# Performance work log

Measured on AMD Instinct MI355X. Metric: run time of the kernel, lower is better.

Reference implementation:

```python
import jax, jax.numpy as jnp
import numpy as np
import math

B, T, D, H = 4, 2048, 1024, 16
DH = D // H

def setup_inputs() -> dict:
    key = jax.random.key(0)
    k1, k2, k3, k4, k5 = jax.random.split(key, 5)
    s = 1.0 / math.sqrt(D)
    x = jax.random.normal(k1, (B, T, D), dtype=jnp.float32)
    # causal mask: 1 where attention allowed (j <= i), 0 elsewhere
    mask = jnp.tril(jnp.ones((T, T), dtype=jnp.float32))[None, None, :, :]
    W_qkv = jax.random.normal(k2, (D, 3 * D), dtype=jnp.float32) * s
    b_qkv = jax.random.normal(k3, (3 * D,), dtype=jnp.float32) * 0.02
    W_proj = jax.random.normal(k4, (D, D), dtype=jnp.float32) * s
    b_proj = jax.random.normal(k5, (D,), dtype=jnp.float32) * 0.02
    return {"x": x, "mask": mask, "W_qkv": W_qkv, "b_qkv": b_qkv,
            "W_proj": W_proj, "b_proj": b_proj}

def reference(x, mask, W_qkv, b_qkv, W_proj, b_proj):
    # qkv: [B,T,3D] -> [3,B,H,T,DH]
    qkv = x @ W_qkv + b_qkv
    qkv = qkv.reshape(B, T, 3, H, DH).transpose(2, 0, 3, 1, 4)
    q, k, v = qkv[0], qkv[1], qkv[2]
    scores = jnp.einsum('bhqd,bhkd->bhqk', q, k) / math.sqrt(DH)
    scores = jnp.where(mask == 0, -jnp.inf, scores)
    attn = jax.nn.softmax(scores, axis=-1)  # dropout p=0 -> identity
    out = jnp.einsum('bhqk,bhkd->bhqd', attn, v)
    out = out.transpose(0, 2, 1, 3).reshape(B, T, D)
    return out @ W_proj + b_proj
```

## Files before the change

### kernel.cpp

```cpp
#include <hip/hip_runtime.h>
#include <hip/hip_bf16.h>

typedef __attribute__((ext_vector_type(8))) short short8;
typedef __attribute__((ext_vector_type(4))) float f32x4;
typedef __attribute__((ext_vector_type(16))) float f32x16;
typedef __attribute__((ext_vector_type(4))) unsigned int u32x4;

#define DEV static __device__ __forceinline__

DEV unsigned short bfc(float f) {
    __bf16 h = (__bf16)f;
    return __builtin_bit_cast(unsigned short, h);
}

DEV unsigned int pack2bf(float lo, float hi) {
    return (unsigned int)bfc(lo) | ((unsigned int)bfc(hi) << 16);
}

DEV void gload16(const void* g, void* l) {
    __builtin_amdgcn_global_load_lds(
        (const __attribute__((address_space(1))) unsigned int*)g,
        (__attribute__((address_space(3))) unsigned int*)l, 16, 0, 0);
}

__global__ void cvt_bf16_kernel(const float* __restrict__ in,
                                unsigned short* __restrict__ out, int n4) {
    int stride = gridDim.x * blockDim.x;
    for (int i = blockIdx.x * blockDim.x + threadIdx.x; i < n4; i += stride) {
        float4 v = reinterpret_cast<const float4*>(in)[i];
        ushort4 o;
        o.x = bfc(v.x); o.y = bfc(v.y); o.z = bfc(v.z); o.w = bfc(v.w);
        reinterpret_cast<ushort4*>(out)[i] = o;
    }
}

__global__ void transpose_cvt_kernel(const float* __restrict__ in,
                                     unsigned short* __restrict__ out,
                                     int K, int N) {
    __shared__ float tile[32][33];
    int n0 = blockIdx.x * 32, k0 = blockIdx.y * 32;
    int tx = threadIdx.x & 31, ty = threadIdx.x >> 5;
    #pragma unroll
    for (int i = 0; i < 32; i += 8)
        tile[ty + i][tx] = in[(size_t)(k0 + ty + i) * N + n0 + tx];
    __syncthreads();
    #pragma unroll
    for (int i = 0; i < 32; i += 8)
        out[(size_t)(n0 + ty + i) * K + k0 + tx] = bfc(tile[tx][ty + i]);
}

template <int EPI>
__global__ __launch_bounds__(256) void gemm_bt(
    const unsigned short* __restrict__ A,
    const unsigned short* __restrict__ Bt,
    const float* __restrict__ bias,
    unsigned short* __restrict__ oQ,
    unsigned short* __restrict__ oK,
    unsigned short* __restrict__ oVt,
    float* __restrict__ oP,
    int M, int N, int K) {
    __shared__ unsigned short As[128 * 32];
    __shared__ unsigned short Bs[128 * 32];
    const int tid = threadIdx.x;
    const int wid = tid >> 6, lane = tid & 63;
    const int r = lane & 15, g = lane >> 4;
    const int wm = wid >> 1, wn = wid & 1;
    const int bm = blockIdx.x, bn = blockIdx.y;

    f32x4 acc[4][4];
    #pragma unroll
    for (int i = 0; i < 4; i++)
        #pragma unroll
        for (int j = 0; j < 4; j++) acc[i][j] = (f32x4)(0.f);

    const int nk = K >> 5;
    for (int kt = 0; kt < nk; ++kt) {
        const int k0 = kt << 5;
        __syncthreads();
        #pragma unroll
        for (int it = 0; it < 2; ++it) {
            int c = it * 256 + wid * 64 + lane;
            int row = c >> 2, cc = c & 3;
            int ccs = cc ^ ((row >> 1) & 3);
            gload16(A + (size_t)(bm * 128 + row) * K + k0 + ccs * 8,
                    (char*)As + (it * 256 + wid * 64) * 16);
            gload16(Bt + (size_t)(bn * 128 + row) * K + k0 + ccs * 8,
                    (char*)Bs + (it * 256 + wid * 64) * 16);
        }
        __syncthreads();
        short8 af[4], bfr[4];
        #pragma unroll
        for (int mi = 0; mi < 4; ++mi) {
            int row = wm * 64 + mi * 16 + r;
            af[mi] = *(const short8*)((const char*)As + row * 64 +
                                      ((g ^ ((row >> 1) & 3)) << 4));
        }
        #pragma unroll
        for (int ni = 0; ni < 4; ++ni) {
            int row = wn * 64 + ni * 16 + r;
            bfr[ni] = *(const short8*)((const char*)Bs + row * 64 +
                                       ((g ^ ((row >> 1) & 3)) << 4));
        }
        #pragma unroll
        for (int mi = 0; mi < 4; ++mi)
            #pragma unroll
            for (int ni = 0; ni < 4; ++ni)
                acc[mi][ni] = __builtin_amdgcn_mfma_f32_16x16x32_bf16(
                    af[mi], bfr[ni], acc[mi][ni], 0, 0, 0);
    }

    const float QSCALE = 0.125f;
    #pragma unroll
    for (int ni = 0; ni < 4; ++ni) {
        int n = bn * 128 + wn * 64 + ni * 16 + r;
        float bb = bias[n];
        #pragma unroll
        for (int mi = 0; mi < 4; ++mi) {
            #pragma unroll
            for (int rr = 0; rr < 4; ++rr) {
                int m = bm * 128 + wm * 64 + mi * 16 + g * 4 + rr;
                float v = acc[mi][ni][rr] + bb;
                if (EPI == 0) {
                    int b = m >> 11, t = m & 2047;
                    int s = n >> 10, hh = (n >> 6) & 15, dh = n & 63;
                    size_t bh = (size_t)(b * 16 + hh);
                    if (s == 0)      oQ[(bh * 2048 + t) * 64 + dh] = bfc(v * QSCALE);
                    else if (s == 1) oK[(bh * 2048 + t) * 64 + dh] = bfc(v);
                    else             oVt[(bh * 64 + dh) * 2048 + t] = bfc(v);
                } else {
                    oP[(size_t)m * N + n] = v;
                }
            }
        }
    }
}

__global__ __launch_bounds__(256) void attn_kernel(
    const unsigned short* __restrict__ Q,
    const unsigned short* __restrict__ Kb,
    const unsigned short* __restrict__ Vt,
    unsigned short* __restrict__ O) {
    __shared__ unsigned short Ks[2 * 64 * 64];
    __shared__ unsigned short Vs[2 * 64 * 64];
    const int tid = threadIdx.x, wid = tid >> 6, lane = tid & 63;
    const int ln31 = lane & 31, hi = lane >> 5;

    const int l = blockIdx.y * 16 + blockIdx.x;
    const int u = l & 255, v = l >> 8;
    const int bh = v * 16 + (u >> 4);
    const int qt = (v & 1) ? (15 - (u & 15)) : (u & 15);

    const size_t hoff = (size_t)bh * 2048 * 64;
    const int qrow0 = qt * 128 + wid * 32;
    const int tq = qrow0 + ln31;
    const float NEG_INF = -__builtin_inff();

    short8 qf[4];
    #pragma unroll
    for (int st = 0; st < 4; ++st)
        qf[st] = *(const short8*)(Q + hoff + (size_t)tq * 64 + st * 16 + hi * 8);

    f32x16 oacc[2];
    oacc[0] = (f32x16)(0.f); oacc[1] = (f32x16)(0.f);
    float mrow = NEG_INF, lrow = 0.f;

    auto stage = [&](int buf, int kvb) {
        #pragma unroll
        for (int it = 0; it < 2; ++it) {
            int c = it * 256 + wid * 64 + lane;
            int row = c >> 3, cc = c & 7;
            int ccs = cc ^ (row & 7);
            gload16(Kb + hoff + (size_t)(kvb + row) * 64 + ccs * 8,
                    (char*)Ks + buf * 8192 + (it * 256 + wid * 64) * 16);
            gload16(Vt + hoff + (size_t)row * 2048 + kvb + ccs * 8,
                    (char*)Vs + buf * 8192 + (it * 256 + wid * 64) * 16);
        }
    };

    const int nkv = 2 * qt + 2;
    stage(0, 0);
    for (int kv = 0; kv < nkv; ++kv) {
        const int kvb = kv * 64;
        const int cur = kv & 1;
        __syncthreads();
        if (kv + 1 < nkv) stage(cur ^ 1, kvb + 64);

        if (kvb <= qrow0) {
            const char* Kbase = (const char*)Ks + cur * 8192;
            const char* Vbase = (const char*)Vs + cur * 8192;
            f32x16 s0 = (f32x16)(0.f), s1 = (f32x16)(0.f);
            #pragma unroll
            for (int st = 0; st < 4; ++st) {
                int row0 = ln31, row1 = 32 + ln31;
                short8 kf0 = *(const short8*)(Kbase + row0 * 128 +
                                              (((2 * st + hi) ^ (row0 & 7)) << 4));
                short8 kf1 = *(const short8*)(Kbase + row1 * 128 +
                                              (((2 * st + hi) ^ (row1 & 7)) << 4));
                s0 = __builtin_amdgcn_mfma_f32_32x32x16_bf16(kf0, qf[st], s0, 0, 0, 0);
                s1 = __builtin_amdgcn_mfma_f32_32x32x16_bf16(kf1, qf[st], s1, 0, 0, 0);
            }
            if (kvb + 63 > qrow0) {
                const int lim = tq - kvb;
                #pragma unroll
                for (int j = 0; j < 16; ++j) {
                    int krel = (j & 3) + 8 * (j >> 2) + 4 * hi;
                    if (krel > lim)      s0[j] = NEG_INF;
                    if (krel + 32 > lim) s1[j] = NEG_INF;
                }
            }
            float mloc = NEG_INF;
            #pragma unroll
            for (int j = 0; j < 16; ++j)
                mloc = fmaxf(mloc, fmaxf(s0[j], s1[j]));
            mloc = fmaxf(mloc, __shfl_xor(mloc, 32));
            float mnew = fmaxf(mrow, mloc);
            float alpha = __expf(mrow - mnew);
            mrow = mnew;
            float ls = 0.f;
            #pragma unroll
            for (int j = 0; j < 16; ++j) {
                float p0 = __expf(s0[j] - mnew);
                float p1 = __expf(s1[j] - mnew);
                s0[j] = p0; s1[j] = p1;
                ls += p0 + p1;
            }
            ls += __shfl_xor(ls, 32);
            lrow = lrow * alpha + ls;
            #pragma unroll
            for (int j = 0; j < 16; ++j) { oacc[0][j] *= alpha; oacc[1][j] *= alpha; }

            #pragma unroll
            for (int m = 0; m < 4; ++m) {
                const int h = m & 1;
                float pa0, pa1, pb0, pb1, pc0, pc1, pd0, pd1;
                if (m < 2) {
                    pa0 = s0[8*h+0]; pa1 = s0[8*h+1]; pc0 = s0[8*h+2]; pc1 = s0[8*h+3];
                    pb0 = s0[8*h+4]; pb1 = s0[8*h+5]; pd0 = s0[8*h+6]; pd1 = s0[8*h+7];
                } else {
                    pa0 = s1[8*h+0]; pa1 = s1[8*h+1]; pc0 = s1[8*h+2]; pc1 = s1[8*h+3];
                    pb0 = s1[8*h+4]; pb1 = s1[8*h+5]; pd0 = s1[8*h+6]; pd1 = s1[8*h+7];
                }
                unsigned int pkA = pack2bf(pa0, pa1), pkC = pack2bf(pc0, pc1);
                unsigned int pkB = pack2bf(pb0, pb1), pkD = pack2bf(pd0, pd1);
                unsigned int oA = __shfl_xor(pkA, 32), oB = __shfl_xor(pkB, 32);
                unsigned int oC = __shfl_xor(pkC, 32), oD = __shfl_xor(pkD, 32);
                u32x4 w;
                w.x = hi ? oB : pkA;
                w.y = hi ? oD : pkC;
                w.z = hi ? pkB : oA;
                w.w = hi ? pkD : oC;
                short8 pfrag = __builtin_bit_cast(short8, w);
                #pragma unroll
                for (int d = 0; d < 2; ++d) {
                    int row = d * 32 + ln31;
                    short8 vf = *(const short8*)(Vbase + row * 128 +
                                                 (((2 * m + hi) ^ (row & 7)) << 4));
                    oacc[d] = __builtin_amdgcn_mfma_f32_32x32x16_bf16(vf, pfrag, oacc[d], 0, 0, 0);
                }
            }
        }
    }

    const int b = bh >> 4, h = bh & 15;
    const float rinv = 1.0f / lrow;
    unsigned short* orow = O + (size_t)(b * 2048 + tq) * 1024 + h * 64;
    #pragma unroll
    for (int d = 0; d < 2; ++d)
        #pragma unroll
        for (int u2 = 0; u2 < 4; ++u2) {
            int dh0 = d * 32 + u2 * 8 + 4 * hi;
            uint2 w;
            w.x = pack2bf(oacc[d][4*u2+0] * rinv, oacc[d][4*u2+1] * rinv);
            w.y = pack2bf(oacc[d][4*u2+2] * rinv, oacc[d][4*u2+3] * rinv);
            *(uint2*)(orow + dh0) = w;
        }
}

extern "C" void kernel_launch(void* const* d_in, const int* in_sizes, int n_in,
                              void* d_out, int out_size, void* d_ws, size_t ws_size,
                              hipStream_t stream) {
    const float* x     = (const float*)d_in[0];
    const float* Wqkv  = (const float*)d_in[2];
    const float* bqkv  = (const float*)d_in[3];
    const float* Wproj = (const float*)d_in[4];
    const float* bproj = (const float*)d_in[5];
    float* out = (float*)d_out;

    char* ws = (char*)d_ws;
    unsigned short* xb  = (unsigned short*)(ws);
    unsigned short* Ob  = (unsigned short*)(ws);
    unsigned short* WqT = (unsigned short*)(ws + (16u << 20));
    unsigned short* WpT = (unsigned short*)(ws + (22u << 20));
    unsigned short* Qb  = (unsigned short*)(ws + (24u << 20));
    unsigned short* Kb  = (unsigned short*)(ws + (40u << 20));
    unsigned short* Vt  = (unsigned short*)(ws + (56u << 20));

    cvt_bf16_kernel<<<2048, 256, 0, stream>>>(x, xb, (8192 * 1024) / 4);
    transpose_cvt_kernel<<<dim3(96, 32), 256, 0, stream>>>(Wqkv, WqT, 1024, 3072);
    transpose_cvt_kernel<<<dim3(32, 32), 256, 0, stream>>>(Wproj, WpT, 1024, 1024);
    gemm_bt<0><<<dim3(64, 24), 256, 0, stream>>>(xb, WqT, bqkv, Qb, Kb, Vt, nullptr,
                                                 8192, 3072, 1024);
    attn_kernel<<<dim3(16, 64), 256, 0, stream>>>(Qb, Kb, Vt, Ob);
    gemm_bt<1><<<dim3(64, 8), 256, 0, stream>>>(Ob, WpT, bproj, nullptr, nullptr,
                                                nullptr, out, 8192, 1024, 1024);
}
```

Baseline: 240.6 us.

## Load K/V fragments directly from global memory, dropping LDS staging and barriers

```diff
diff --git a/kernel.cpp b/kernel.cpp
--- a/kernel.cpp
+++ b/kernel.cpp
@@ -140,8 +140,6 @@
     const unsigned short* __restrict__ Kb,
     const unsigned short* __restrict__ Vt,
     unsigned short* __restrict__ O) {
-    __shared__ unsigned short Ks[2 * 64 * 64];
-    __shared__ unsigned short Vs[2 * 64 * 64];
     const int tid = threadIdx.x, wid = tid >> 6, lane = tid & 63;
     const int ln31 = lane & 31, hi = lane >> 5;
 
@@ -164,100 +162,91 @@
     oacc[0] = (f32x16)(0.f); oacc[1] = (f32x16)(0.f);
     float mrow = NEG_INF, lrow = 0.f;
 
-    auto stage = [&](int buf, int kvb) {
-        #pragma unroll
-        for (int it = 0; it < 2; ++it) {
-            int c = it * 256 + wid * 64 + lane;
-            int row = c >> 3, cc = c & 7;
-            int ccs = cc ^ (row & 7);
-            gload16(Kb + hoff + (size_t)(kvb + row) * 64 + ccs * 8,
-                    (char*)Ks + buf * 8192 + (it * 256 + wid * 64) * 16);
-            gload16(Vt + hoff + (size_t)row * 2048 + kvb + ccs * 8,
-                    (char*)Vs + buf * 8192 + (it * 256 + wid * 64) * 16);
-        }
-    };
-
-    const int nkv = 2 * qt + 2;
-    stage(0, 0);
-    for (int kv = 0; kv < nkv; ++kv) {
+    const unsigned short* Kh = Kb + hoff;
+    const unsigned short* Vh = Vt + hoff;
+
+    const int nt = 2 * qt + (wid >> 1) + 1;
+    for (int kv = 0; kv < nt; ++kv) {
         const int kvb = kv * 64;
-        const int cur = kv & 1;
-        __syncthreads();
-        if (kv + 1 < nkv) stage(cur ^ 1, kvb + 64);
-
-        if (kvb <= qrow0) {
-            const char* Kbase = (const char*)Ks + cur * 8192;
-            const char* Vbase = (const char*)Vs + cur * 8192;
-            f32x16 s0 = (f32x16)(0.f), s1 = (f32x16)(0.f);
-            #pragma unroll
-            for (int st = 0; st < 4; ++st) {
-                int row0 = ln31, row1 = 32 + ln31;
-                short8 kf0 = *(const short8*)(Kbase + row0 * 128 +
-                                              (((2 * st + hi) ^ (row0 & 7)) << 4));
-                short8 kf1 = *(const short8*)(Kbase + row1 * 128 +
-                                              (((2 * st + hi) ^ (row1 & 7)) << 4));
-                s0 = __builtin_amdgcn_mfma_f32_32x32x16_bf16(kf0, qf[st], s0, 0, 0, 0);
-                s1 = __builtin_amdgcn_mfma_f32_32x32x16_bf16(kf1, qf[st], s1, 0, 0, 0);
+
+        const unsigned short* Kp = Kh + (size_t)kvb * 64;
+        short8 kf0[4], kf1[4];
+        #pragma unroll
+        for (int st = 0; st < 4; ++st) {
+            kf0[st] = *(const short8*)(Kp + ln31 * 64 + st * 16 + hi * 8);
+            kf1[st] = *(const short8*)(Kp + (32 + ln31) * 64 + st * 16 + hi * 8);
+        }
+
+        f32x16 s0 = (f32x16)(0.f), s1 = (f32x16)(0.f);
+        #pragma unroll
+        for (int st = 0; st < 4; ++st) {
+            s0 = __builtin_amdgcn_mfma_f32_32x32x16_bf16(kf0[st], qf[st], s0, 0, 0, 0);
+            s1 = __builtin_amdgcn_mfma_f32_32x32x16_bf16(kf1[st], qf[st], s1, 0, 0, 0);
+        }
+
+        short8 vf[4][2];
+        #pragma unroll
+        for (int m = 0; m < 4; ++m)
+            #pragma unroll
+            for (int d = 0; d < 2; ++d)
+                vf[m][d] = *(const short8*)(Vh + (size_t)(d * 32 + ln31) * 2048 +
+                                            kvb + m * 16 + hi * 8);
+
+        if (kvb + 63 > qrow0) {
+            const int lim = tq - kvb;
+            #pragma unroll
+            for (int j = 0; j < 16; ++j) {
+                int krel = (j & 3) + 8 * (j >> 2) + 4 * hi;
+                if (krel > lim)      s0[j] = NEG_INF;
+                if (krel + 32 > lim) s1[j] = NEG_INF;
             }
-            if (kvb + 63 > qrow0) {
-                const int lim = tq - kvb;
-                #pragma unroll
-                for (int j = 0; j < 16; ++j) {
-                    int krel = (j & 3) + 8 * (j >> 2) + 4 * hi;
-                    if (krel > lim)      s0[j] = NEG_INF;
-                    if (krel + 32 > lim) s1[j] = NEG_INF;
-                }
+        }
+
+        float mloc = NEG_INF;
+        #pragma unroll
+        for (int j = 0; j < 16; ++j)
+            mloc = fmaxf(mloc, fmaxf(s0[j], s1[j]));
+        mloc = fmaxf(mloc, __shfl_xor(mloc, 32));
+        float mnew = fmaxf(mrow, mloc);
+        float alpha = __expf(mrow - mnew);
+        mrow = mnew;
+        float ls = 0.f;
+        #pragma unroll
+        for (int j = 0; j < 16; ++j) {
+            float p0 = __expf(s0[j] - mnew);
+            float p1 = __expf(s1[j] - mnew);
+            s0[j] = p0; s1[j] = p1;
+            ls += p0 + p1;
+        }
+        ls += __shfl_xor(ls, 32);
+        lrow = lrow * alpha + ls;
+        #pragma unroll
+        for (int j = 0; j < 16; ++j) { oacc[0][j] *= alpha; oacc[1][j] *= alpha; }
+
+        #pragma unroll
+        for (int m = 0; m < 4; ++m) {
+            const int h = m & 1;
+            float pa0, pa1, pb0, pb1, pc0, pc1, pd0, pd1;
+            if (m < 2) {
+                pa0 = s0[8*h+0]; pa1 = s0[8*h+1]; pc0 = s0[8*h+2]; pc1 = s0[8*h+3];
+                pb0 = s0[8*h+4]; pb1 = s0[8*h+5]; pd0 = s0[8*h+6]; pd1 = s0[8*h+7];
+            } else {
+                pa0 = s1[8*h+0]; pa1 = s1[8*h+1]; pc0 = s1[8*h+2]; pc1 = s1[8*h+3];
+                pb0 = s1[8*h+4]; pb1 = s1[8*h+5]; pd0 = s1[8*h+6]; pd1 = s1[8*h+7];
             }
-            float mloc = NEG_INF;
-            #pragma unroll
-            for (int j = 0; j < 16; ++j)
-                mloc = fmaxf(mloc, fmaxf(s0[j], s1[j]));
-            mloc = fmaxf(mloc, __shfl_xor(mloc, 32));
-            float mnew = fmaxf(mrow, mloc);
-            float alpha = __expf(mrow - mnew);
-            mrow = mnew;
-            float ls = 0.f;
-            #pragma unroll
-            for (int j = 0; j < 16; ++j) {
-                float p0 = __expf(s0[j] - mnew);
-                float p1 = __expf(s1[j] - mnew);
-                s0[j] = p0; s1[j] = p1;
-                ls += p0 + p1;
-            }
-            ls += __shfl_xor(ls, 32);
-            lrow = lrow * alpha + ls;
-            #pragma unroll
-            for (int j = 0; j < 16; ++j) { oacc[0][j] *= alpha; oacc[1][j] *= alpha; }
-
-            #pragma unroll
-            for (int m = 0; m < 4; ++m) {
-                const int h = m & 1;
-                float pa0, pa1, pb0, pb1, pc0, pc1, pd0, pd1;
-                if (m < 2) {
-                    pa0 = s0[8*h+0]; pa1 = s0[8*h+1]; pc0 = s0[8*h+2]; pc1 = s0[8*h+3];
-                    pb0 = s0[8*h+4]; pb1 = s0[8*h+5]; pd0 = s0[8*h+6]; pd1 = s0[8*h+7];
-                } else {
-                    pa0 = s1[8*h+0]; pa1 = s1[8*h+1]; pc0 = s1[8*h+2]; pc1 = s1[8*h+3];
-                    pb0 = s1[8*h+4]; pb1 = s1[8*h+5]; pd0 = s1[8*h+6]; pd1 = s1[8*h+7];
-                }
-                unsigned int pkA = pack2bf(pa0, pa1), pkC = pack2bf(pc0, pc1);
-                unsigned int pkB = pack2bf(pb0, pb1), pkD = pack2bf(pd0, pd1);
-                unsigned int oA = __shfl_xor(pkA, 32), oB = __shfl_xor(pkB, 32);
-                unsigned int oC = __shfl_xor(pkC, 32), oD = __shfl_xor(pkD, 32);
-                u32x4 w;
-                w.x = hi ? oB : pkA;
-                w.y = hi ? oD : pkC;
-                w.z = hi ? pkB : oA;
-                w.w = hi ? pkD : oC;
-                short8 pfrag = __builtin_bit_cast(short8, w);
-                #pragma unroll
-                for (int d = 0; d < 2; ++d) {
-                    int row = d * 32 + ln31;
-                    short8 vf = *(const short8*)(Vbase + row * 128 +
-                                                 (((2 * m + hi) ^ (row & 7)) << 4));
-                    oacc[d] = __builtin_amdgcn_mfma_f32_32x32x16_bf16(vf, pfrag, oacc[d], 0, 0, 0);
-                }
-            }
+            unsigned int pkA = pack2bf(pa0, pa1), pkC = pack2bf(pc0, pc1);
+            unsigned int pkB = pack2bf(pb0, pb1), pkD = pack2bf(pd0, pd1);
+            unsigned int oA = __shfl_xor(pkA, 32), oB = __shfl_xor(pkB, 32);
+            unsigned int oC = __shfl_xor(pkC, 32), oD = __shfl_xor(pkD, 32);
+            u32x4 w;
+            w.x = hi ? oB : pkA;
+            w.y = hi ? oD : pkC;
+            w.z = hi ? pkB : oA;
+            w.w = hi ? pkD : oC;
+            short8 pfrag = __builtin_bit_cast(short8, w);
+            #pragma unroll
+            for (int d = 0; d < 2; ++d)
+                oacc[d] = __builtin_amdgcn_mfma_f32_32x32x16_bf16(vf[m][d], pfrag, oacc[d], 0, 0, 0);
         }
     }
 
```

Result: slower. 275.1 us (+14.3%).
